# Optimization experiments

Hardware: AMD Instinct MI355X
Metric: run time of the kernel (lower is better)

## Reference

```python
import jax, jax.numpy as jnp
import numpy as np

BN_EPS = 1e-5
K = 3  # kernel_size
G = 4  # num_groups


def setup_inputs() -> dict:
    key = jax.random.key(0)
    ks = jax.random.split(key, 8)
    B, C, H, W = 16, 192, 96, 96
    R = C // 4
    return {
        "x": jax.random.normal(ks[0], (B, C, H, W), jnp.float32),
        "cam_w1": jax.random.normal(ks[1], (R, C), jnp.float32) * 0.05,
        "cam_w2": jax.random.normal(ks[2], (C, R), jnp.float32) * 0.05,
        "proj_w1": jax.random.normal(ks[3], (R, C), jnp.float32) * 0.05,
        "bn_gamma": jnp.ones((R,), jnp.float32),
        "bn_beta": jnp.zeros((R,), jnp.float32),
        "proj_w2": jax.random.normal(ks[4], (G * C, R), jnp.float32) * 0.05,
        "adk_weight": jax.random.normal(ks[5], (G, C, K, K), jnp.float32) * 0.02,
    }


def reference(x, cam_w1, cam_w2, proj_w1, bn_gamma, bn_beta, proj_w2, adk_weight):
    B, C, H, W = x.shape

    # ---- CAM: theta = sigmoid(fc(avgpool1(x)) + fc(maxpool1(x))) -> [B, C]
    def fc(v):  # v: [B, C]
        h = jax.nn.relu(v @ cam_w1.T)  # [B, C//4]
        return h @ cam_w2.T            # [B, C]

    avg = x.mean(axis=(2, 3))
    mx = x.max(axis=(2, 3))
    theta = jax.nn.sigmoid(fc(avg) + fc(mx))  # [B, C]

    # ---- AdaptiveDynamicKernel: dynamic per-(sample,channel) 3x3 filters
    # AdaptiveAvgPool2d(3): H, W divisible by 3 -> uniform pooling
    pooled = x.reshape(B, C, K, H // K, K, W // K).mean(axis=(3, 5))  # [B,C,3,3]
    h = jnp.einsum('bchw,rc->brhw', pooled, proj_w1)  # [B, C//4, 3, 3]
    # BatchNorm2d (eval, running_mean=0, running_var=1)
    scale_bn = bn_gamma / jnp.sqrt(1.0 + BN_EPS)
    h = jax.nn.relu(h * scale_bn[None, :, None, None] + bn_beta[None, :, None, None])
    s = jnp.einsum('brhw,or->bohw', h, proj_w2)  # [B, G*C, 3, 3]
    s = s.reshape(B, G, C, K, K)
    s = jax.nn.softmax(s, axis=1)
    weight = jnp.sum(s * adk_weight[None], axis=1)  # [B, C, 3, 3]

    # ---- central-difference correction
    w_sum = weight.sum(axis=(2, 3))         # [B, C]
    w_center = weight[:, :, K // 2, K // 2]  # [B, C]
    delta = w_sum - theta * w_center
    weight_s = weight.at[:, :, K // 2, K // 2].add(-delta)

    # ---- grouped depthwise conv, groups = B*C
    kernel = weight_s.reshape(B * C, 1, K, K)
    xin = x.reshape(1, B * C, H, W)
    out = jax.lax.conv_general_dilated(
        xin, kernel,
        window_strides=(1, 1),
        padding=[(K // 2, K // 2), (K // 2, K // 2)],
        dimension_numbers=('NCHW', 'OIHW', 'NCHW'),
        feature_group_count=B * C,
    )
    return out.reshape(B, C, H, W)
```

## Files before the change

### kernel.cpp

```cpp
#include <hip/hip_runtime.h>
#include <math.h>

#define CCH   192
#define RCH   48
#define NB    16
#define HW    9216
#define BCTOT (NB*CCH)

__global__ __launch_bounds__(256) void k_stats(const float* __restrict__ x,
                                               float* __restrict__ avg,
                                               float* __restrict__ mx,
                                               float* __restrict__ pooled)
{
    int bc = blockIdx.x;
    const float4* p4 = (const float4*)(x + (size_t)bc * HW);
    int t = threadIdx.x;
    float ps[9];
    float m = -INFINITY;
#pragma unroll
    for (int k = 0; k < 9; ++k) {
        int kr = k / 3, kc = k % 3;
        int row = kr * 32 + (t >> 3);
        int wq  = kc * 8  + (t & 7);
        float4 v = p4[row * 24 + wq];
        ps[k] = v.x + v.y + v.z + v.w;
        m = fmaxf(m, fmaxf(fmaxf(v.x, v.y), fmaxf(v.z, v.w)));
    }
#pragma unroll
    for (int off = 32; off > 0; off >>= 1) {
#pragma unroll
        for (int k = 0; k < 9; ++k) ps[k] += __shfl_down(ps[k], off);
        m = fmaxf(m, __shfl_down(m, off));
    }
    __shared__ float red[4][10];
    int wid = t >> 6, lane = t & 63;
    if (lane == 0) {
#pragma unroll
        for (int k = 0; k < 9; ++k) red[wid][k] = ps[k];
        red[wid][9] = m;
    }
    __syncthreads();
    if (t == 0) {
        float tot = 0.f;
#pragma unroll
        for (int k = 0; k < 9; ++k) {
            float pk = red[0][k] + red[1][k] + red[2][k] + red[3][k];
            pooled[bc * 9 + k] = pk * (1.0f / 1024.0f);
            tot += pk;
        }
        float mm = fmaxf(fmaxf(red[0][9], red[1][9]),
                         fmaxf(red[2][9], red[3][9]));
        avg[bc] = tot * (1.0f / (float)HW);
        mx[bc]  = mm;
    }
}

__global__ __launch_bounds__(256) void k_theta_hh(
    const float* __restrict__ avg, const float* __restrict__ mx,
    const float* __restrict__ pooled,
    const float* __restrict__ cam_w1, const float* __restrict__ cam_w2,
    const float* __restrict__ proj_w1,
    const float* __restrict__ bn_gamma, const float* __restrict__ bn_beta,
    float* __restrict__ theta, float* __restrict__ hh)
{
    int b = blockIdx.x;
    int t = threadIdx.x;
    __shared__ float s_av[CCH], s_mx[CCH], s_pool[CCH * 9], s_h1p[96], s_h1[RCH];
    if (t < CCH) { s_av[t] = avg[b * CCH + t]; s_mx[t] = mx[b * CCH + t]; }
    for (int i = t; i < CCH * 9; i += 256) s_pool[i] = pooled[b * CCH * 9 + i];
    __syncthreads();
    if (t < 96) {
        int r = t % 48, sel = t / 48;
        const float* src = sel ? s_mx : s_av;
        const float* w = cam_w1 + r * CCH;
        float acc = 0.f;
        for (int c = 0; c < CCH; ++c) acc += src[c] * w[c];
        s_h1p[sel * 48 + r] = fmaxf(acc, 0.f);
    }
    __syncthreads();
    if (t < RCH) s_h1[t] = s_h1p[t] + s_h1p[48 + t];
    __syncthreads();
    if (t < CCH) {
        const float* w = cam_w2 + t * RCH;
        float acc = 0.f;
        for (int r = 0; r < RCH; ++r) acc += s_h1[r] * w[r];
        theta[b * CCH + t] = 1.0f / (1.0f + expf(-acc));
    }
    float bn_s = 1.0f / sqrtf(1.0f + 1e-5f);
    for (int i = t; i < RCH * 9; i += 256) {
        int r = i / 9, k = i % 9;
        const float* w = proj_w1 + r * CCH;
        float acc = 0.f;
        for (int c = 0; c < CCH; ++c) acc += s_pool[c * 9 + k] * w[c];
        float val = acc * (bn_gamma[r] * bn_s) + bn_beta[r];
        hh[b * RCH * 9 + i] = fmaxf(val, 0.f);
    }
}

__global__ __launch_bounds__(256) void k_weight(
    const float* __restrict__ hh, const float* __restrict__ proj_w2,
    const float* __restrict__ adk, float* __restrict__ wgt)
{
    int gid = blockIdx.x * 256 + threadIdx.x;
    if (gid >= BCTOT * 9) return;
    int b = gid / (CCH * 9);
    int rem = gid % (CCH * 9);
    int c = rem / 9, k = rem % 9;
    const float* hv = hh + b * RCH * 9 + k;
    float sg[4];
#pragma unroll
    for (int g = 0; g < 4; ++g) {
        const float* w = proj_w2 + (size_t)(g * CCH + c) * RCH;
        float acc = 0.f;
        for (int r = 0; r < RCH; ++r) acc += hv[r * 9] * w[r];
        sg[g] = acc;
    }
    float mxv = fmaxf(fmaxf(sg[0], sg[1]), fmaxf(sg[2], sg[3]));
    float e[4];
    float sum = 0.f;
#pragma unroll
    for (int g = 0; g < 4; ++g) { e[g] = expf(sg[g] - mxv); sum += e[g]; }
    float inv = 1.0f / sum;
    float acc = 0.f;
#pragma unroll
    for (int g = 0; g < 4; ++g)
        acc += (e[g] * inv) * adk[(size_t)(g * CCH + c) * 9 + k];
    wgt[gid] = acc;
}

__global__ __launch_bounds__(256) void k_conv(
    const float* __restrict__ x, const float* __restrict__ wgt,
    const float* __restrict__ theta, float* __restrict__ out)
{
    int gid = blockIdx.x * 256 + threadIdx.x;
    int plane = gid / 192;
    int sub   = gid % 192;
    int rg = sub / 24, wq = sub % 24;
    int r0 = rg * 12;
    int w0 = wq * 4;

    float wr[9];
    float wsum = 0.f;
#pragma unroll
    for (int k = 0; k < 9; ++k) { wr[k] = wgt[plane * 9 + k]; wsum += wr[k]; }
    float th = theta[plane];
    wr[4] = wr[4] * (1.f + th) - wsum;

    const float* p = x + (size_t)plane * HW;
    float* o = out + (size_t)plane * HW;

    float acc[3][4];
#pragma unroll
    for (int i = 0; i <= 13; ++i) {
        int r = r0 - 1 + i;
        float win[6];
        bool inr = (r >= 0) && (r < 96);
        const float* prow = p + r * 96;
        if (inr) {
            float4 a = ((const float4*)prow)[wq];
            win[0] = (wq > 0)  ? prow[w0 - 1] : 0.f;
            win[1] = a.x; win[2] = a.y; win[3] = a.z; win[4] = a.w;
            win[5] = (wq < 23) ? prow[w0 + 4] : 0.f;
        } else {
#pragma unroll
            for (int j = 0; j < 6; ++j) win[j] = 0.f;
        }
        if (i <= 11) {
#pragma unroll
            for (int j = 0; j < 4; ++j)
                acc[i % 3][j] = wr[0] * win[j] + wr[1] * win[j + 1] + wr[2] * win[j + 2];
        }
        if (i >= 1 && i <= 12) {
#pragma unroll
            for (int j = 0; j < 4; ++j)
                acc[(i - 1) % 3][j] += wr[3] * win[j] + wr[4] * win[j + 1] + wr[5] * win[j + 2];
        }
        if (i >= 2) {
            const int s = (i - 2) % 3;
#pragma unroll
            for (int j = 0; j < 4; ++j)
                acc[s][j] += wr[6] * win[j] + wr[7] * win[j + 1] + wr[8] * win[j + 2];
            float4 o4;
            o4.x = acc[s][0]; o4.y = acc[s][1]; o4.z = acc[s][2]; o4.w = acc[s][3];
            ((float4*)(o + (size_t)(r - 1) * 96))[wq] = o4;
        }
    }
}

extern "C" void kernel_launch(void* const* d_in, const int* in_sizes, int n_in,
                              void* d_out, int out_size, void* d_ws, size_t ws_size,
                              hipStream_t stream) {
    const float* x        = (const float*)d_in[0];
    const float* cam_w1   = (const float*)d_in[1];
    const float* cam_w2   = (const float*)d_in[2];
    const float* proj_w1  = (const float*)d_in[3];
    const float* bn_gamma = (const float*)d_in[4];
    const float* bn_beta  = (const float*)d_in[5];
    const float* proj_w2  = (const float*)d_in[6];
    const float* adk      = (const float*)d_in[7];
    float* out = (float*)d_out;
    float* ws  = (float*)d_ws;

    float* avg    = ws;
    float* mx     = ws + 3072;
    float* pooled = ws + 6144;
    float* theta  = ws + 33792;
    float* hh     = ws + 36864;
    float* wgt    = ws + 43776;

    k_stats   <<<BCTOT, 256, 0, stream>>>(x, avg, mx, pooled);
    k_theta_hh<<<NB,    256, 0, stream>>>(avg, mx, pooled, cam_w1, cam_w2,
                                          proj_w1, bn_gamma, bn_beta, theta, hh);
    k_weight  <<<(BCTOT * 9) / 256, 256, 0, stream>>>(hh, proj_w2, adk, wgt);
    k_conv    <<<(BCTOT * 192) / 256, 256, 0, stream>>>(x, wgt, theta, out);
}
```

Measured before the change: 85.46 us.

## Fuse weight generation into coefficient kernel and widen conv tiles with shuffle halos

Merges the per-sample weight-generation kernel into the theta/hidden kernel, keeping the hidden activations in shared memory and removing one launch plus a global round trip. Only 16 blocks now compute all 27648 weights, so that stage runs with much less parallelism. The depthwise conv maps one wavefront per plane, and each lane handles 12 rows by 12 columns using three float4 loads. Halo columns come from lane shuffles instead of extra scalar global loads, at the cost of more registers per thread and fewer threads overall.

```diff
diff --git a/kernel.cpp b/kernel.cpp
--- a/kernel.cpp
+++ b/kernel.cpp
@@ -55,17 +55,19 @@
     }
 }
 
-__global__ __launch_bounds__(256) void k_theta_hh(
+__global__ __launch_bounds__(256) void k_coeff(
     const float* __restrict__ avg, const float* __restrict__ mx,
     const float* __restrict__ pooled,
     const float* __restrict__ cam_w1, const float* __restrict__ cam_w2,
     const float* __restrict__ proj_w1,
     const float* __restrict__ bn_gamma, const float* __restrict__ bn_beta,
-    float* __restrict__ theta, float* __restrict__ hh)
+    const float* __restrict__ proj_w2, const float* __restrict__ adk,
+    float* __restrict__ theta, float* __restrict__ wgt)
 {
     int b = blockIdx.x;
     int t = threadIdx.x;
-    __shared__ float s_av[CCH], s_mx[CCH], s_pool[CCH * 9], s_h1p[96], s_h1[RCH];
+    __shared__ float s_av[CCH], s_mx[CCH], s_pool[CCH * 9];
+    __shared__ float s_h1p[96], s_h1[RCH], s_hh[RCH * 9];
     if (t < CCH) { s_av[t] = avg[b * CCH + t]; s_mx[t] = mx[b * CCH + t]; }
     for (int i = t; i < CCH * 9; i += 256) s_pool[i] = pooled[b * CCH * 9 + i];
     __syncthreads();
@@ -93,51 +95,42 @@
         float acc = 0.f;
         for (int c = 0; c < CCH; ++c) acc += s_pool[c * 9 + k] * w[c];
         float val = acc * (bn_gamma[r] * bn_s) + bn_beta[r];
-        hh[b * RCH * 9 + i] = fmaxf(val, 0.f);
-    }
-}
-
-__global__ __launch_bounds__(256) void k_weight(
-    const float* __restrict__ hh, const float* __restrict__ proj_w2,
-    const float* __restrict__ adk, float* __restrict__ wgt)
-{
-    int gid = blockIdx.x * 256 + threadIdx.x;
-    if (gid >= BCTOT * 9) return;
-    int b = gid / (CCH * 9);
-    int rem = gid % (CCH * 9);
-    int c = rem / 9, k = rem % 9;
-    const float* hv = hh + b * RCH * 9 + k;
-    float sg[4];
-#pragma unroll
-    for (int g = 0; g < 4; ++g) {
-        const float* w = proj_w2 + (size_t)(g * CCH + c) * RCH;
-        float acc = 0.f;
-        for (int r = 0; r < RCH; ++r) acc += hv[r * 9] * w[r];
-        sg[g] = acc;
-    }
-    float mxv = fmaxf(fmaxf(sg[0], sg[1]), fmaxf(sg[2], sg[3]));
-    float e[4];
-    float sum = 0.f;
-#pragma unroll
-    for (int g = 0; g < 4; ++g) { e[g] = expf(sg[g] - mxv); sum += e[g]; }
-    float inv = 1.0f / sum;
-    float acc = 0.f;
-#pragma unroll
-    for (int g = 0; g < 4; ++g)
-        acc += (e[g] * inv) * adk[(size_t)(g * CCH + c) * 9 + k];
-    wgt[gid] = acc;
+        s_hh[i] = fmaxf(val, 0.f);
+    }
+    __syncthreads();
+    for (int i = t; i < CCH * 9; i += 256) {
+        int c = i / 9, k = i % 9;
+        float sg[4];
+#pragma unroll
+        for (int g = 0; g < 4; ++g) {
+            const float* w = proj_w2 + (size_t)(g * CCH + c) * RCH;
+            float acc = 0.f;
+            for (int r = 0; r < RCH; ++r) acc += s_hh[r * 9 + k] * w[r];
+            sg[g] = acc;
+        }
+        float mxv = fmaxf(fmaxf(sg[0], sg[1]), fmaxf(sg[2], sg[3]));
+        float e[4];
+        float sum = 0.f;
+#pragma unroll
+        for (int g = 0; g < 4; ++g) { e[g] = expf(sg[g] - mxv); sum += e[g]; }
+        float inv = 1.0f / sum;
+        float acc = 0.f;
+#pragma unroll
+        for (int g = 0; g < 4; ++g)
+            acc += (e[g] * inv) * adk[(size_t)(g * CCH + c) * 9 + k];
+        wgt[b * CCH * 9 + i] = acc;
+    }
 }
 
 __global__ __launch_bounds__(256) void k_conv(
     const float* __restrict__ x, const float* __restrict__ wgt,
     const float* __restrict__ theta, float* __restrict__ out)
 {
-    int gid = blockIdx.x * 256 + threadIdx.x;
-    int plane = gid / 192;
-    int sub   = gid % 192;
-    int rg = sub / 24, wq = sub % 24;
-    int r0 = rg * 12;
-    int w0 = wq * 4;
+    int t = threadIdx.x;
+    int wid = t >> 6, lane = t & 63;
+    int plane = blockIdx.x * 4 + wid;
+    int rg = lane >> 3, cs = lane & 7;
+    int rbase = rg * 12 - 1;
 
     float wr[9];
     float wsum = 0.f;
@@ -146,43 +139,51 @@
     float th = theta[plane];
     wr[4] = wr[4] * (1.f + th) - wsum;
 
-    const float* p = x + (size_t)plane * HW;
-    float* o = out + (size_t)plane * HW;
-
-    float acc[3][4];
+    const float4* p4 = (const float4*)(x + (size_t)plane * HW);
+    float4* o4p = (float4*)(out + (size_t)plane * HW);
+
+    float acc[3][12];
 #pragma unroll
     for (int i = 0; i <= 13; ++i) {
-        int r = r0 - 1 + i;
-        float win[6];
+        int r = rbase + i;
         bool inr = (r >= 0) && (r < 96);
-        const float* prow = p + r * 96;
+        float4 a0, a1, a2;
         if (inr) {
-            float4 a = ((const float4*)prow)[wq];
-            win[0] = (wq > 0)  ? prow[w0 - 1] : 0.f;
-            win[1] = a.x; win[2] = a.y; win[3] = a.z; win[4] = a.w;
-            win[5] = (wq < 23) ? prow[w0 + 4] : 0.f;
+            const float4* prow = p4 + r * 24 + cs * 3;
+            a0 = prow[0]; a1 = prow[1]; a2 = prow[2];
         } else {
-#pragma unroll
-            for (int j = 0; j < 6; ++j) win[j] = 0.f;
-        }
+            a0 = make_float4(0.f, 0.f, 0.f, 0.f);
+            a1 = a0; a2 = a0;
+        }
+        float lv = __shfl_up(a2.w, 1);
+        float rv = __shfl_down(a0.x, 1);
+        float w[14];
+        w[0] = (cs == 0) ? 0.f : lv;
+        w[1] = a0.x; w[2] = a0.y; w[3] = a0.z; w[4] = a0.w;
+        w[5] = a1.x; w[6] = a1.y; w[7] = a1.z; w[8] = a1.w;
+        w[9] = a2.x; w[10] = a2.y; w[11] = a2.z; w[12] = a2.w;
+        w[13] = (cs == 7) ? 0.f : rv;
+
         if (i <= 11) {
 #pragma unroll
-            for (int j = 0; j < 4; ++j)
-                acc[i % 3][j] = wr[0] * win[j] + wr[1] * win[j + 1] + wr[2] * win[j + 2];
+            for (int j = 0; j < 12; ++j)
+                acc[i % 3][j] = wr[0] * w[j] + wr[1] * w[j + 1] + wr[2] * w[j + 2];
         }
         if (i >= 1 && i <= 12) {
 #pragma unroll
-            for (int j = 0; j < 4; ++j)
-                acc[(i - 1) % 3][j] += wr[3] * win[j] + wr[4] * win[j + 1] + wr[5] * win[j + 2];
+            for (int j = 0; j < 12; ++j)
+                acc[(i - 1) % 3][j] += wr[3] * w[j] + wr[4] * w[j + 1] + wr[5] * w[j + 2];
         }
         if (i >= 2) {
             const int s = (i - 2) % 3;
 #pragma unroll
-            for (int j = 0; j < 4; ++j)
-                acc[s][j] += wr[6] * win[j] + wr[7] * win[j + 1] + wr[8] * win[j + 2];
-            float4 o4;
-            o4.x = acc[s][0]; o4.y = acc[s][1]; o4.z = acc[s][2]; o4.w = acc[s][3];
-            ((float4*)(o + (size_t)(r - 1) * 96))[wq] = o4;
+            for (int j = 0; j < 12; ++j)
+                acc[s][j] += wr[6] * w[j] + wr[7] * w[j + 1] + wr[8] * w[j + 2];
+            int orow = rbase + i - 1;
+            float4* od = o4p + orow * 24 + cs * 3;
+            od[0] = make_float4(acc[s][0], acc[s][1], acc[s][2], acc[s][3]);
+            od[1] = make_float4(acc[s][4], acc[s][5], acc[s][6], acc[s][7]);
+            od[2] = make_float4(acc[s][8], acc[s][9], acc[s][10], acc[s][11]);
         }
     }
 }
@@ -205,12 +206,11 @@
     float* mx     = ws + 3072;
     float* pooled = ws + 6144;
     float* theta  = ws + 33792;
-    float* hh     = ws + 36864;
-    float* wgt    = ws + 43776;
-
-    k_stats   <<<BCTOT, 256, 0, stream>>>(x, avg, mx, pooled);
-    k_theta_hh<<<NB,    256, 0, stream>>>(avg, mx, pooled, cam_w1, cam_w2,
-                                          proj_w1, bn_gamma, bn_beta, theta, hh);
-    k_weight  <<<(BCTOT * 9) / 256, 256, 0, stream>>>(hh, proj_w2, adk, wgt);
-    k_conv    <<<(BCTOT * 192) / 256, 256, 0, stream>>>(x, wgt, theta, out);
-}
+    float* wgt    = ws + 36864;
+
+    k_stats <<<BCTOT, 256, 0, stream>>>(x, avg, mx, pooled);
+    k_coeff <<<NB,    256, 0, stream>>>(avg, mx, pooled, cam_w1, cam_w2,
+                                        proj_w1, bn_gamma, bn_beta,
+                                        proj_w2, adk, theta, wgt);
+    k_conv  <<<BCTOT / 4, 256, 0, stream>>>(x, wgt, theta, out);
+}
```

Result: slower. 95.34 us (+11.6%).

## Widen conv thread tiles, add nontemporal stores, and restructure stats reduction

Applied to the files above, without the earlier changes.

The depthwise conv now gives each thread an 8-wide column strip instead of a 4-wide one, which halves the thread count and the halo loads per output. Outputs are written with nontemporal stores so the output stream does not evict x from cache. The stats kernel now uses 576 threads, one wavefront per pooling cell, so each wave needs only one shuffle reduction instead of nine. The wider strip raises register use per thread and cuts the number of waves available to hide memory latency.

```diff
diff --git a/kernel.cpp b/kernel.cpp
--- a/kernel.cpp
+++ b/kernel.cpp
@@ -7,55 +7,52 @@
 #define HW    9216
 #define BCTOT (NB*CCH)
 
-__global__ __launch_bounds__(256) void k_stats(const float* __restrict__ x,
+typedef float f32x4 __attribute__((ext_vector_type(4)));
+
+__device__ inline void st_nt4(float* p, float a, float b, float c, float d) {
+    f32x4 v; v.x = a; v.y = b; v.z = c; v.w = d;
+    __builtin_nontemporal_store(v, (f32x4*)p);
+}
+
+__global__ __launch_bounds__(576) void k_stats(const float* __restrict__ x,
                                                float* __restrict__ avg,
                                                float* __restrict__ mx,
                                                float* __restrict__ pooled)
 {
     int bc = blockIdx.x;
+    int t = threadIdx.x;
+    int w = t >> 6, l = t & 63;
+    int kr = w / 3, kc = w % 3;
     const float4* p4 = (const float4*)(x + (size_t)bc * HW);
-    int t = threadIdx.x;
-    float ps[9];
-    float m = -INFINITY;
-#pragma unroll
-    for (int k = 0; k < 9; ++k) {
-        int kr = k / 3, kc = k % 3;
-        int row = kr * 32 + (t >> 3);
-        int wq  = kc * 8  + (t & 7);
-        float4 v = p4[row * 24 + wq];
-        ps[k] = v.x + v.y + v.z + v.w;
-        m = fmaxf(m, fmaxf(fmaxf(v.x, v.y), fmaxf(v.z, v.w)));
-    }
+    int row = kr * 32 + (l >> 1);
+    int c0  = kc * 8 + (l & 1) * 4;
+    const float4* pr = p4 + row * 24 + c0;
+    float4 v0 = pr[0], v1 = pr[1], v2 = pr[2], v3 = pr[3];
+    float s = (v0.x + v0.y + v0.z + v0.w) + (v1.x + v1.y + v1.z + v1.w)
+            + (v2.x + v2.y + v2.z + v2.w) + (v3.x + v3.y + v3.z + v3.w);
+    float m = fmaxf(fmaxf(fmaxf(v0.x, v0.y), fmaxf(v0.z, v0.w)),
+             fmaxf(fmaxf(fmaxf(v1.x, v1.y), fmaxf(v1.z, v1.w)),
+             fmaxf(fmaxf(fmaxf(v2.x, v2.y), fmaxf(v2.z, v2.w)),
+                   fmaxf(fmaxf(v3.x, v3.y), fmaxf(v3.z, v3.w)))));
 #pragma unroll
     for (int off = 32; off > 0; off >>= 1) {
-#pragma unroll
-        for (int k = 0; k < 9; ++k) ps[k] += __shfl_down(ps[k], off);
+        s += __shfl_down(s, off);
         m = fmaxf(m, __shfl_down(m, off));
     }
-    __shared__ float red[4][10];
-    int wid = t >> 6, lane = t & 63;
-    if (lane == 0) {
-#pragma unroll
-        for (int k = 0; k < 9; ++k) red[wid][k] = ps[k];
-        red[wid][9] = m;
-    }
-    __syncthreads();
+    __shared__ float ls[9], lm[9];
+    if (l == 0) { ls[w] = s; lm[w] = m; }
+    __syncthreads();
+    if (t < 9) pooled[bc * 9 + t] = ls[t] * (1.0f / 1024.0f);
     if (t == 0) {
-        float tot = 0.f;
-#pragma unroll
-        for (int k = 0; k < 9; ++k) {
-            float pk = red[0][k] + red[1][k] + red[2][k] + red[3][k];
-            pooled[bc * 9 + k] = pk * (1.0f / 1024.0f);
-            tot += pk;
-        }
-        float mm = fmaxf(fmaxf(red[0][9], red[1][9]),
-                         fmaxf(red[2][9], red[3][9]));
+        float tot = 0.f, mm = -INFINITY;
+#pragma unroll
+        for (int k = 0; k < 9; ++k) { tot += ls[k]; mm = fmaxf(mm, lm[k]); }
         avg[bc] = tot * (1.0f / (float)HW);
         mx[bc]  = mm;
     }
 }
 
-__global__ __launch_bounds__(256) void k_theta_hh(
+__global__ __launch_bounds__(256) void k_coeff1(
     const float* __restrict__ avg, const float* __restrict__ mx,
     const float* __restrict__ pooled,
     const float* __restrict__ cam_w1, const float* __restrict__ cam_w2,
@@ -97,7 +94,7 @@
     }
 }
 
-__global__ __launch_bounds__(256) void k_weight(
+__global__ __launch_bounds__(256) void k_coeff2(
     const float* __restrict__ hh, const float* __restrict__ proj_w2,
     const float* __restrict__ adk, float* __restrict__ wgt)
 {
@@ -133,11 +130,10 @@
     const float* __restrict__ theta, float* __restrict__ out)
 {
     int gid = blockIdx.x * 256 + threadIdx.x;
-    int plane = gid / 192;
-    int sub   = gid % 192;
-    int rg = sub / 24, wq = sub % 24;
+    int plane = gid / 96;
+    int sub   = gid % 96;
+    int rg = sub / 12, cp = sub % 12;
     int r0 = rg * 12;
-    int w0 = wq * 4;
 
     float wr[9];
     float wsum = 0.f;
@@ -147,42 +143,50 @@
     wr[4] = wr[4] * (1.f + th) - wsum;
 
     const float* p = x + (size_t)plane * HW;
+    const float4* p4 = (const float4*)p;
     float* o = out + (size_t)plane * HW;
 
-    float acc[3][4];
+    float acc[3][8];
 #pragma unroll
     for (int i = 0; i <= 13; ++i) {
         int r = r0 - 1 + i;
-        float win[6];
         bool inr = (r >= 0) && (r < 96);
-        const float* prow = p + r * 96;
+        float4 a, b;
+        float lh, rh;
         if (inr) {
-            float4 a = ((const float4*)prow)[wq];
-            win[0] = (wq > 0)  ? prow[w0 - 1] : 0.f;
-            win[1] = a.x; win[2] = a.y; win[3] = a.z; win[4] = a.w;
-            win[5] = (wq < 23) ? prow[w0 + 4] : 0.f;
+            const float4* pr = p4 + r * 24 + 2 * cp;
+            a = pr[0]; b = pr[1];
+            lh = (cp > 0)  ? p[r * 96 + 8 * cp - 1] : 0.f;
+            rh = (cp < 11) ? p[r * 96 + 8 * cp + 8] : 0.f;
         } else {
-#pragma unroll
-            for (int j = 0; j < 6; ++j) win[j] = 0.f;
-        }
+            a = make_float4(0.f, 0.f, 0.f, 0.f);
+            b = a; lh = 0.f; rh = 0.f;
+        }
+        float win[10];
+        win[0] = lh;
+        win[1] = a.x; win[2] = a.y; win[3] = a.z; win[4] = a.w;
+        win[5] = b.x; win[6] = b.y; win[7] = b.z; win[8] = b.w;
+        win[9] = rh;
+
         if (i <= 11) {
 #pragma unroll
-            for (int j = 0; j < 4; ++j)
+            for (int j = 0; j < 8; ++j)
                 acc[i % 3][j] = wr[0] * win[j] + wr[1] * win[j + 1] + wr[2] * win[j + 2];
         }
         if (i >= 1 && i <= 12) {
 #pragma unroll
-            for (int j = 0; j < 4; ++j)
+            for (int j = 0; j < 8; ++j)
                 acc[(i - 1) % 3][j] += wr[3] * win[j] + wr[4] * win[j + 1] + wr[5] * win[j + 2];
         }
         if (i >= 2) {
             const int s = (i - 2) % 3;
 #pragma unroll
-            for (int j = 0; j < 4; ++j)
+            for (int j = 0; j < 8; ++j)
                 acc[s][j] += wr[6] * win[j] + wr[7] * win[j + 1] + wr[8] * win[j + 2];
-            float4 o4;
-            o4.x = acc[s][0]; o4.y = acc[s][1]; o4.z = acc[s][2]; o4.w = acc[s][3];
-            ((float4*)(o + (size_t)(r - 1) * 96))[wq] = o4;
+            int orow = r0 + i - 2;
+            float* od = o + orow * 96 + 8 * cp;
+            st_nt4(od,     acc[s][0], acc[s][1], acc[s][2], acc[s][3]);
+            st_nt4(od + 4, acc[s][4], acc[s][5], acc[s][6], acc[s][7]);
         }
     }
 }
@@ -208,9 +212,9 @@
     float* hh     = ws + 36864;
     float* wgt    = ws + 43776;
 
-    k_stats   <<<BCTOT, 256, 0, stream>>>(x, avg, mx, pooled);
-    k_theta_hh<<<NB,    256, 0, stream>>>(avg, mx, pooled, cam_w1, cam_w2,
-                                          proj_w1, bn_gamma, bn_beta, theta, hh);
-    k_weight  <<<(BCTOT * 9) / 256, 256, 0, stream>>>(hh, proj_w2, adk, wgt);
-    k_conv    <<<(BCTOT * 192) / 256, 256, 0, stream>>>(x, wgt, theta, out);
-}
+    k_stats  <<<BCTOT, 576, 0, stream>>>(x, avg, mx, pooled);
+    k_coeff1 <<<NB,    256, 0, stream>>>(avg, mx, pooled, cam_w1, cam_w2,
+                                         proj_w1, bn_gamma, bn_beta, theta, hh);
+    k_coeff2 <<<(BCTOT * 9) / 256, 256, 0, stream>>>(hh, proj_w2, adk, wgt);
+    k_conv   <<<(BCTOT * 96) / 256, 256, 0, stream>>>(x, wgt, theta, out);
+}
```

New measurement: 87.94 us. +2.9%, slower.
